# Kernel optimization log

Hardware: AMD Instinct MI355X
Metric: run time of the kernel (lower is better)

The kernel has to match this reference:

```python
import jax, jax.numpy as jnp
import numpy as np

RADIUS = [3, 3, 4, 4]
DILATION = [1, 2, 1, 2]
N_HEAD = 4
D_K = 8
SCALE = 1.0 / np.sqrt(8.0)  # module hardcodes sqrt(8)


def _patches(a, r, d):
    # a: (b, t, c, h, w) -> (b, t, c, ls2, h, w), dilated (2r+1)x(2r+1) window,
    # zero padding (invalid positions masked separately).
    b, t, c, h, w = a.shape
    p = r * d
    ap = jnp.pad(a, ((0, 0), (0, 0), (0, 0), (p, p), (p, p)))
    ls = 2 * r + 1
    sl = [ap[..., dy * d:dy * d + h, dx * d:dx * d + w]
          for dy in range(ls) for dx in range(ls)]
    return jnp.stack(sl, axis=3)


def _valid_mask(h, w, r, d):
    # (ls2, h, w) bool: True where window position is inside the image
    m = _patches(jnp.ones((1, 1, 1, h, w)), r, d)
    return m[0, 0, 0] > 0.5


def _head_attn(q, k, v, r, d):
    # q,k,v: (b, t, c, h, w); attention over all t' frames x local window
    b, t, c, h, w = q.shape
    kp = _patches(k, r, d)        # (b, t', c, p, h, w)
    vp = _patches(v, r, d)
    valid = _valid_mask(h, w, r, d)  # (p, h, w)
    e = jnp.einsum('btchw,bscphw->btsphw', q, kp) * SCALE
    e = jnp.where(valid[None, None, None], e, -jnp.inf)  # OOB -> -inf like CUDA kernel
    e = e.reshape(b, t, t * valid.shape[0], h, w)
    attn = jax.nn.softmax(e, axis=2).reshape(b, t, t, -1, h, w)
    return jnp.einsum('btsphw,bscphw->btchw', attn, vp)


def setup_inputs() -> dict:
    key = jax.random.key(0)
    kx, kq, kk, kv, ko = jax.random.split(key, 5)
    C = 32
    std = 1.0 / np.sqrt(C)
    x = jax.random.normal(kx, (2, 5, C, 64, 64), dtype=jnp.float32)
    Wq = jax.random.normal(kq, (N_HEAD * D_K, C), dtype=jnp.float32) * std
    Wk = jax.random.normal(kk, (N_HEAD * D_K, C), dtype=jnp.float32) * std
    Wv = jax.random.normal(kv, (N_HEAD * D_K, C), dtype=jnp.float32) * std
    Wo = jax.random.normal(ko, (C, C), dtype=jnp.float32) * std
    return {"x": x, "Wq": Wq, "Wk": Wk, "Wv": Wv, "Wo": Wo}


def reference(x, Wq, Wk, Wv, Wo):
    # 1x1x1 Conv3d == per-pixel channel matmul
    q = jnp.einsum('btchw,kc->btkhw', x, Wq)
    k = jnp.einsum('btchw,kc->btkhw', x, Wk)
    v = jnp.einsum('btchw,kc->btkhw', x, Wv)
    outs = []
    for i in range(N_HEAD):
        s = slice(i * D_K, (i + 1) * D_K)
        outs.append(_head_attn(q[:, :, s], k[:, :, s], v[:, :, s],
                               RADIUS[i], DILATION[i]))
    out = jnp.concatenate(outs, axis=2)
    out = jnp.einsum('btchw,kc->btkhw', out, Wo)
    return out + x
```

## Files before the change

### kernel.cpp

```cpp
#include <hip/hip_runtime.h>
#include <stdint.h>

#define NT 5
#define NC 32
#define NH 4
#define HW 4096
#define NPIX 40960
#define QS 0.51006972789f
#define EBIAS 12.0f
#define NINF (-__builtin_inff())

typedef _Float16 half_t;
typedef half_t h2 __attribute__((ext_vector_type(2)));

static __device__ __forceinline__ h2 as_h2(uint32_t u) {
  union { uint32_t u; h2 h; } c; c.u = u; return c.h;
}
static __device__ __forceinline__ uint32_t pack_h2(float a, float b) {
  union { h2 h; uint32_t u; } c;
  c.h.x = (half_t)a; c.h.y = (half_t)b;
  return c.u;
}

#if __has_builtin(__builtin_amdgcn_exp2f)
#define EXP2(x) __builtin_amdgcn_exp2f(x)
#else
#define EXP2(x) exp2f(x)
#endif

static __device__ __forceinline__ float dot8i(const uint4& a, const uint4& b, float c) {
#if __has_builtin(__builtin_amdgcn_fdot2)
  c = __builtin_amdgcn_fdot2(as_h2(a.x), as_h2(b.x), c, false);
  c = __builtin_amdgcn_fdot2(as_h2(a.y), as_h2(b.y), c, false);
  c = __builtin_amdgcn_fdot2(as_h2(a.z), as_h2(b.z), c, false);
  c = __builtin_amdgcn_fdot2(as_h2(a.w), as_h2(b.w), c, false);
  return c;
#else
  const h2 a0 = as_h2(a.x), a1 = as_h2(a.y), a2 = as_h2(a.z), a3 = as_h2(a.w);
  const h2 b0 = as_h2(b.x), b1 = as_h2(b.y), b2 = as_h2(b.z), b3 = as_h2(b.w);
  c = fmaf((float)a0.x, (float)b0.x, c);
  c = fmaf((float)a0.y, (float)b0.y, c);
  c = fmaf((float)a1.x, (float)b1.x, c);
  c = fmaf((float)a1.y, (float)b1.y, c);
  c = fmaf((float)a2.x, (float)b2.x, c);
  c = fmaf((float)a2.y, (float)b2.y, c);
  c = fmaf((float)a3.x, (float)b3.x, c);
  c = fmaf((float)a3.y, (float)b3.y, c);
  return c;
#endif
}

__global__ __launch_bounds__(256) void qkv_kernel(
    const float* __restrict__ x,
    const float* __restrict__ Wq, const float* __restrict__ Wk,
    const float* __restrict__ Wv,
    uint2* __restrict__ qf, uint2* __restrict__ kf, uint2* __restrict__ vf)
{
  const int p   = blockIdx.x * 256 + threadIdx.x;
  const int by  = blockIdx.y;
  const int h   = by >> 1;
  const int jg  = by & 1;
  const int bt  = p >> 12;
  const int pix = p & 4095;

  const float* xp = x + (size_t)bt * (NC * HW) + pix;
  float xc[NC];
  #pragma unroll
  for (int c = 0; c < NC; ++c) xc[c] = xp[(size_t)c * HW];

  float qv[4], kv4[4], vv4[4];
  #pragma unroll
  for (int j = 0; j < 4; ++j) {
    const int o = h * 8 + jg * 4 + j;
    float aq = 0.f, ak = 0.f, av = 0.f;
    #pragma unroll
    for (int c = 0; c < NC; ++c) {
      const float xv = xc[c];
      aq = fmaf(xv, Wq[o * NC + c], aq);
      ak = fmaf(xv, Wk[o * NC + c], ak);
      av = fmaf(xv, Wv[o * NC + c], av);
    }
    qv[j] = aq * QS; kv4[j] = ak; vv4[j] = av;
  }
  const size_t base = (((size_t)bt * NH + h) * HW + pix) * 2 + jg;
  uint2 qq, kk, vv;
  qq.x = pack_h2(qv[0], qv[1]);  qq.y = pack_h2(qv[2], qv[3]);
  kk.x = pack_h2(kv4[0], kv4[1]); kk.y = pack_h2(kv4[2], kv4[3]);
  vv.x = pack_h2(vv4[0], vv4[1]); vv.y = pack_h2(vv4[2], vv4[3]);
  qf[base] = qq;
  kf[base] = kk;
  vf[base] = vv;
}

template <int R, int D>
static __device__ __forceinline__ void attn_body(
    int b, int t, int h, int s, int yb,
    const uint4* __restrict__ qf, const uint4* __restrict__ kf,
    const uint4* __restrict__ vf,
    uint4* __restrict__ pa, float* __restrict__ pl,
    uint4* __restrict__ k_lds, uint4* __restrict__ v_lds)
{
  constexpr int LS    = 2 * R + 1;
  constexpr int NROWS = 8 + 2 * R;
  const int tid  = threadIdx.x;
  const int w    = tid >> 6;
  const int lane = tid & 63;

  const int y0 = (D == 1) ? (yb * 8) : ((yb & 1) + 2 * ((yb >> 1) * 8));

  const uint4* kg = kf + (size_t)((b * NT + s) * NH + h) * HW;
  const uint4* vg = vf + (size_t)((b * NT + s) * NH + h) * HW;
  for (int idx = tid; idx < NROWS * 64; idx += 256) {
    const int r  = idx >> 6, xs = idx & 63;
    int ys = y0 + (r - R) * D;
    ys = ys < 0 ? 0 : (ys > 63 ? 63 : ys);
    const int pos = (D == 1) ? xs : ((xs & 1) * 32 + (xs >> 1));
    k_lds[r * 64 + pos] = kg[ys * 64 + xs];
    v_lds[r * 64 + pos] = vg[ys * 64 + xs];
  }
  __syncthreads();

  const int xp = lane >> 5;
  const int cb = (D == 1) ? lane : (lane & 31);
  const int x  = (D == 1) ? lane : (2 * (lane & 31) + xp);
  const int yA = y0 + 2 * w * D;
  const int yB = yA + D;
  const int pixA = yA * 64 + x, pixB = yB * 64 + x;

  const uint4* qp = qf + (size_t)((b * NT + t) * NH + h) * HW;
  const uint4 qA = qp[pixA];
  const uint4 qB = qp[pixB];

  int   posArr[LS];
  float eoArr[LS];
  #pragma unroll
  for (int i = 0; i < LS; ++i) {
    const int  cx  = cb + i - R;
    const bool okx = (unsigned)cx < (D == 1 ? 64u : 32u);
    const int  cc  = okx ? cx : 0;
    posArr[i] = (D == 1) ? cc : (xp * 32 + cc);
    eoArr[i]  = okx ? 0.f : NINF;
  }

  float lA = 0.f, lB = 0.f;
  h2 aA[4], aB[4];
  const h2 z2 = { (half_t)0.f, (half_t)0.f };
  #pragma unroll
  for (int i = 0; i < 4; ++i) { aA[i] = z2; aB[i] = z2; }

  #pragma unroll 2
  for (int u = 0; u <= LS; ++u) {
    const int ykey = y0 + (2 * w + u - R) * D;
    const bool oky = (unsigned)ykey < 64u;
    const bool okA = (u < LS) && oky;
    const bool okB = (u > 0)  && oky;
    if (!(okA || okB)) continue;
    const float biA = okA ? -EBIAS : NINF;
    const float biB = okB ? -EBIAS : NINF;
    const uint4* kr = k_lds + (2 * w + u) * 64;
    const uint4* vr = v_lds + (2 * w + u) * 64;

    uint4 kbuf[2], vbuf[2];
    #pragma unroll
    for (int i = 0; i < 2; ++i) {
      kbuf[i] = kr[posArr[i]];
      vbuf[i] = vr[posArr[i]];
    }
    #pragma unroll
    for (int i = 0; i < LS; ++i) {
      const uint4 kk = kbuf[i & 1];
      const uint4 vv = vbuf[i & 1];
      if (i + 2 < LS) {
        kbuf[i & 1] = kr[posArr[i + 2]];
        vbuf[i & 1] = vr[posArr[i + 2]];
      }
      const float ciA = biA + eoArr[i];
      const float ciB = biB + eoArr[i];
      const float pA = EXP2(dot8i(qA, kk, ciA));
      const float pB = EXP2(dot8i(qB, kk, ciB));
      lA += pA; lB += pB;
      const half_t pAh = (half_t)pA, pBh = (half_t)pB;
      const h2 pA2 = { pAh, pAh }, pB2 = { pBh, pBh };
      const h2 w0 = as_h2(vv.x), w1 = as_h2(vv.y), w2 = as_h2(vv.z), w3 = as_h2(vv.w);
      aA[0] += pA2 * w0; aA[1] += pA2 * w1; aA[2] += pA2 * w2; aA[3] += pA2 * w3;
      aB[0] += pB2 * w0; aB[1] += pB2 * w1; aB[2] += pB2 * w2; aB[3] += pB2 * w3;
    }
  }

  const size_t plane = (size_t)(s * NH + h) * NPIX + (size_t)(b * NT + t) * HW;
  union { h2 hh[4]; uint4 u; } cA, cB;
  #pragma unroll
  for (int i = 0; i < 4; ++i) { cA.hh[i] = aA[i]; cB.hh[i] = aB[i]; }
  pa[plane + pixA] = cA.u;
  pa[plane + pixB] = cB.u;
  pl[plane + pixA] = lA;
  pl[plane + pixB] = lB;
}

__global__ __launch_bounds__(256) void attn_kernel(
    const uint4* __restrict__ qf, const uint4* __restrict__ kf,
    const uint4* __restrict__ vf, uint4* __restrict__ pa, float* __restrict__ pl)
{
  __shared__ uint4 k_lds[16 * 64];
  __shared__ uint4 v_lds[16 * 64];
  const int bid = blockIdx.x;
  int h, rest;
  if (bid < 800) { h = 2 + (bid & 1); rest = bid >> 1; }
  else           { h = ((bid - 800) & 1); rest = (bid - 800) >> 1; }
  const int yb = rest & 7; rest >>= 3;
  const int s  = rest % 5;
  const int bt = rest / 5;
  const int t = bt % NT, b = bt / NT;
  if      (h == 0) attn_body<3, 1>(b, t, 0, s, yb, qf, kf, vf, pa, pl, k_lds, v_lds);
  else if (h == 1) attn_body<3, 2>(b, t, 1, s, yb, qf, kf, vf, pa, pl, k_lds, v_lds);
  else if (h == 2) attn_body<4, 1>(b, t, 2, s, yb, qf, kf, vf, pa, pl, k_lds, v_lds);
  else             attn_body<4, 2>(b, t, 3, s, yb, qf, kf, vf, pa, pl, k_lds, v_lds);
}

__global__ __launch_bounds__(256) void proj_kernel(
    const uint4* __restrict__ pa, const float* __restrict__ pl,
    const float* __restrict__ x, const float* __restrict__ Wo,
    float* __restrict__ out)
{
  const int p   = blockIdx.x * 256 + threadIdx.x;
  const int og  = blockIdx.y;
  const int bt  = p >> 12;
  const int pix = p & 4095;

  float oc[32];
  #pragma unroll
  for (int h = 0; h < NH; ++h) {
    float a[8], l = 0.f;
    #pragma unroll
    for (int i = 0; i < 8; ++i) a[i] = 0.f;
    #pragma unroll
    for (int s = 0; s < NT; ++s) {
      const size_t plane = (size_t)(s * NH + h) * NPIX + p;
      const uint4 v = pa[plane];
      l += pl[plane];
      const h2 v0 = as_h2(v.x), v1 = as_h2(v.y), v2 = as_h2(v.z), v3 = as_h2(v.w);
      a[0] += (float)v0.x; a[1] += (float)v0.y;
      a[2] += (float)v1.x; a[3] += (float)v1.y;
      a[4] += (float)v2.x; a[5] += (float)v2.y;
      a[6] += (float)v3.x; a[7] += (float)v3.y;
    }
    const float inv = 1.0f / l;
    #pragma unroll
    for (int i = 0; i < 8; ++i) oc[h * 8 + i] = a[i] * inv;
  }

  const float* xpt = x + (size_t)bt * (NC * HW) + pix;
  float* yp = out + (size_t)bt * (NC * HW) + pix;
  #pragma unroll
  for (int oo = 0; oo < 4; ++oo) {
    const int o = og * 4 + oo;
    float acc = xpt[(size_t)o * HW];
    #pragma unroll
    for (int c = 0; c < NC; ++c)
      acc = fmaf(oc[c], Wo[o * NC + c], acc);
    yp[(size_t)o * HW] = acc;
  }
}

extern "C" void kernel_launch(void* const* d_in, const int* in_sizes, int n_in,
                              void* d_out, int out_size, void* d_ws, size_t ws_size,
                              hipStream_t stream)
{
  const float* x  = (const float*)d_in[0];
  const float* Wq = (const float*)d_in[1];
  const float* Wk = (const float*)d_in[2];
  const float* Wv = (const float*)d_in[3];
  const float* Wo = (const float*)d_in[4];

  char* ws = (char*)d_ws;
  uint2* qf = (uint2*)ws;
  uint2* kf = (uint2*)(ws + 2621440);
  uint2* vf = (uint2*)(ws + 2 * 2621440);
  uint4* pa = (uint4*)(ws + 3 * 2621440);
  float* pl = (float*)(ws + 3 * 2621440 + 13107200);

  qkv_kernel<<<dim3(160, 8), 256, 0, stream>>>(x, Wq, Wk, Wv, qf, kf, vf);
  attn_kernel<<<1600, 256, 0, stream>>>((const uint4*)qf, (const uint4*)kf,
                                        (const uint4*)vf, pa, pl);
  proj_kernel<<<dim3(160, 8), 256, 0, stream>>>(pa, pl, x, Wo, (float*)d_out);
}
```

Before: 111.6 us.

## Stage input tiles in LDS to share loads across output groups in qkv and proj

The QKV and output-projection kernels now load a 64-pixel tile of inputs (x channels, or the partial attention sums and normalisers) into shared memory once per block. Four wavefront groups then compute different output channel groups from that shared tile. Previously each blockIdx.y slice re-read the same inputs from global memory, giving 8x redundant traffic. The cost is LDS staging plus a barrier, and the grid reshapes to 640x2 blocks.

```diff
diff --git a/kernel.cpp b/kernel.cpp
--- a/kernel.cpp
+++ b/kernel.cpp
@@ -56,37 +56,47 @@
     const float* __restrict__ Wv,
     uint2* __restrict__ qf, uint2* __restrict__ kf, uint2* __restrict__ vf)
 {
-  const int p   = blockIdx.x * 256 + threadIdx.x;
-  const int by  = blockIdx.y;
-  const int h   = by >> 1;
-  const int jg  = by & 1;
-  const int bt  = p >> 12;
-  const int pix = p & 4095;
-
-  const float* xp = x + (size_t)bt * (NC * HW) + pix;
-  float xc[NC];
-  #pragma unroll
-  for (int c = 0; c < NC; ++c) xc[c] = xp[(size_t)c * HW];
-
-  float qv[4], kv4[4], vv4[4];
-  #pragma unroll
-  for (int j = 0; j < 4; ++j) {
-    const int o = h * 8 + jg * 4 + j;
-    float aq = 0.f, ak = 0.f, av = 0.f;
-    #pragma unroll
-    for (int c = 0; c < NC; ++c) {
-      const float xv = xc[c];
-      aq = fmaf(xv, Wq[o * NC + c], aq);
-      ak = fmaf(xv, Wk[o * NC + c], ak);
-      av = fmaf(xv, Wv[o * NC + c], av);
+  __shared__ float xl[NC][64];
+  const int tile = blockIdx.x;
+  const int by   = blockIdx.y;
+  const int bt   = tile >> 6;
+  const int pix0 = (tile & 63) * 64;
+  const int tid  = threadIdx.x;
+
+  const float* xp = x + (size_t)bt * (NC * HW) + pix0;
+  for (int i = tid; i < NC * 64; i += 256) {
+    const int c = i >> 6, p = i & 63;
+    xl[c][p] = xp[(size_t)c * HW + p];
+  }
+  __syncthreads();
+
+  const int p  = tid & 63;
+  const int g  = tid >> 6;
+  const int h  = by * 2 + (g >> 1);
+  const int jg = g & 1;
+
+  float aq[4], ak[4], av[4];
+  #pragma unroll
+  for (int j = 0; j < 4; ++j) { aq[j] = 0.f; ak[j] = 0.f; av[j] = 0.f; }
+  const int o0 = h * 8 + jg * 4;
+  #pragma unroll
+  for (int c = 0; c < NC; ++c) {
+    const float xv = xl[c][p];
+    #pragma unroll
+    for (int j = 0; j < 4; ++j) {
+      aq[j] = fmaf(xv, Wq[(o0 + j) * NC + c], aq[j]);
+      ak[j] = fmaf(xv, Wk[(o0 + j) * NC + c], ak[j]);
+      av[j] = fmaf(xv, Wv[(o0 + j) * NC + c], av[j]);
     }
-    qv[j] = aq * QS; kv4[j] = ak; vv4[j] = av;
-  }
-  const size_t base = (((size_t)bt * NH + h) * HW + pix) * 2 + jg;
+  }
+  #pragma unroll
+  for (int j = 0; j < 4; ++j) aq[j] *= QS;
+
+  const size_t base = (((size_t)bt * NH + h) * HW + pix0 + p) * 2 + jg;
   uint2 qq, kk, vv;
-  qq.x = pack_h2(qv[0], qv[1]);  qq.y = pack_h2(qv[2], qv[3]);
-  kk.x = pack_h2(kv4[0], kv4[1]); kk.y = pack_h2(kv4[2], kv4[3]);
-  vv.x = pack_h2(vv4[0], vv4[1]); vv.y = pack_h2(vv4[2], vv4[3]);
+  qq.x = pack_h2(aq[0], aq[1]); qq.y = pack_h2(aq[2], aq[3]);
+  kk.x = pack_h2(ak[0], ak[1]); kk.y = pack_h2(ak[2], ak[3]);
+  vv.x = pack_h2(av[0], av[1]); vv.y = pack_h2(av[2], av[3]);
   qf[base] = qq;
   kf[base] = kk;
   vf[base] = vv;
@@ -222,10 +232,24 @@
     const float* __restrict__ x, const float* __restrict__ Wo,
     float* __restrict__ out)
 {
-  const int p   = blockIdx.x * 256 + threadIdx.x;
-  const int og  = blockIdx.y;
-  const int bt  = p >> 12;
-  const int pix = p & 4095;
+  __shared__ uint4 pal[20][64];
+  __shared__ float pll[20][64];
+  const int tile = blockIdx.x;
+  const int by   = blockIdx.y;
+  const int bt   = tile >> 6;
+  const int pix0 = (tile & 63) * 64;
+  const int tid  = threadIdx.x;
+
+  const size_t btp = (size_t)bt * HW + pix0;
+  for (int i = tid; i < 20 * 64; i += 256) {
+    const int pe = i >> 6, p = i & 63;
+    pal[pe][p] = pa[(size_t)pe * NPIX + btp + p];
+    pll[pe][p] = pl[(size_t)pe * NPIX + btp + p];
+  }
+  __syncthreads();
+
+  const int p = tid & 63;
+  const int g = tid >> 6;
 
   float oc[32];
   #pragma unroll
@@ -235,9 +259,8 @@
     for (int i = 0; i < 8; ++i) a[i] = 0.f;
     #pragma unroll
     for (int s = 0; s < NT; ++s) {
-      const size_t plane = (size_t)(s * NH + h) * NPIX + p;
-      const uint4 v = pa[plane];
-      l += pl[plane];
+      const uint4 v = pal[s * NH + h][p];
+      l += pll[s * NH + h][p];
       const h2 v0 = as_h2(v.x), v1 = as_h2(v.y), v2 = as_h2(v.z), v3 = as_h2(v.w);
       a[0] += (float)v0.x; a[1] += (float)v0.y;
       a[2] += (float)v1.x; a[3] += (float)v1.y;
@@ -249,11 +272,12 @@
     for (int i = 0; i < 8; ++i) oc[h * 8 + i] = a[i] * inv;
   }
 
-  const float* xpt = x + (size_t)bt * (NC * HW) + pix;
-  float* yp = out + (size_t)bt * (NC * HW) + pix;
+  const float* xpt = x + (size_t)bt * (NC * HW) + pix0 + p;
+  float* yp = out + (size_t)bt * (NC * HW) + pix0 + p;
+  const int o0 = by * 16 + g * 4;
   #pragma unroll
   for (int oo = 0; oo < 4; ++oo) {
-    const int o = og * 4 + oo;
+    const int o = o0 + oo;
     float acc = xpt[(size_t)o * HW];
     #pragma unroll
     for (int c = 0; c < NC; ++c)
@@ -279,8 +303,8 @@
   uint4* pa = (uint4*)(ws + 3 * 2621440);
   float* pl = (float*)(ws + 3 * 2621440 + 13107200);
 
-  qkv_kernel<<<dim3(160, 8), 256, 0, stream>>>(x, Wq, Wk, Wv, qf, kf, vf);
+  qkv_kernel<<<dim3(640, 2), 256, 0, stream>>>(x, Wq, Wk, Wv, qf, kf, vf);
   attn_kernel<<<1600, 256, 0, stream>>>((const uint4*)qf, (const uint4*)kf,
                                         (const uint4*)vf, pa, pl);
-  proj_kernel<<<dim3(160, 8), 256, 0, stream>>>(pa, pl, x, Wo, (float*)d_out);
-}
+  proj_kernel<<<dim3(640, 2), 256, 0, stream>>>(pa, pl, x, Wo, (float*)d_out);
+}
```

Result: slower. 125.4 us (+12.3%).
